# Kernel tuning notes

Measured on AMD Instinct MI355X. Metric: run time of the kernel, lower is better.

## Reference

```python
import jax, jax.numpy as jnp
import numpy as np

# NF4 codebook (bitsandbytes normal-float-4 values)
NF4 = jnp.asarray(np.array([
    -1.0, -0.6961928009986877, -0.5250730514526367, -0.39491748809814453,
    -0.28444138169288635, -0.18477343022823334, -0.09105003625154495, 0.0,
    0.07958029955625534, 0.16093020141124725, 0.24611230194568634, 0.33791524171829224,
    0.44070982933044434, 0.5626170039176941, 0.7229568362236023, 1.0], dtype=np.float32))

BLOCK = 64         # bnb nf4 blocksize
SCALING = 2.0      # alpha / r = 128 / 64
OUT, IN = 4096, 4096

def dequantize_nf4(codes, absmax):
    # codes: [out, in] int32 in [0,16); absmax: [out*in/BLOCK] per-block scale
    vals = NF4[codes].reshape(-1, BLOCK)           # [n_blocks, BLOCK]
    w = vals * absmax[:, None]                     # blockwise rescale
    return w.reshape(OUT, IN)                      # [out, in]

def setup_inputs() -> dict:
    key = jax.random.key(0)
    k1, k2, k3, k4, k5 = jax.random.split(key, 5)
    x = jax.random.normal(k1, (4, 2048, 4096), dtype=jnp.float32)
    lora_A = jax.random.normal(k2, (64, 4096), dtype=jnp.float32) * 0.02
    lora_B = jax.random.normal(k3, (4096, 64), dtype=jnp.float32) * 0.02
    absmax = jax.random.uniform(k4, (4096 * 4096 // BLOCK,), dtype=jnp.float32) * 0.1
    qweight_codes = jax.random.randint(k5, (4096, 4096), 0, 16, dtype=jnp.int32)
    return {"x": x, "lora_A": lora_A, "lora_B": lora_B,
            "absmax": absmax, "qweight_codes": qweight_codes}

def reference(x, lora_A, lora_B, absmax, qweight_codes):
    # LinearForward, quantized nf4 path, no dora/bone, dropout disabled (eval):
    # F.linear(x, W) + scaling * F.linear(F.linear(x, lora_A), lora_B)
    W = dequantize_nf4(qweight_codes, absmax)              # [out, in]
    base = jnp.einsum('btd,od->bto', x, W)                 # base GEMM
    lora = jnp.einsum('btr,or->bto', jnp.einsum('btd,rd->btr', x, lora_A), lora_B)
    return base + SCALING * lora
```

## Files before the change

kernel.cpp:

```cpp
#include <hip/hip_runtime.h>


typedef _Float16 half8 __attribute__((ext_vector_type(8)));
typedef float f32x4 __attribute__((ext_vector_type(4)));

#define M_DIM 8192
#define N_DIM 4096
#define K_DIM 4096

__constant__ float NF4C[16] = {
    -1.0f, -0.6961928009986877f, -0.5250730514526367f, -0.39491748809814453f,
    -0.28444138169288635f, -0.18477343022823334f, -0.09105003625154495f, 0.0f,
    0.07958029955625534f, 0.16093020141124725f, 0.24611230194568634f, 0.33791524171829224f,
    0.44070982933044434f, 0.5626170039176941f, 0.7229568362236023f, 1.0f};

__device__ __forceinline__ void gl16(void* lds, const void* g) {
  __builtin_amdgcn_global_load_lds(
      (const __attribute__((address_space(1))) void*)g,
      (__attribute__((address_space(3))) void*)lds, 16, 0, 0);
}

__global__ __launch_bounds__(256) void prep_x(const float4* __restrict__ x,
                                              half8* __restrict__ xh) {
  size_t i = (size_t)blockIdx.x * 256 + threadIdx.x;
  float4 a = x[2 * i];
  float4 b = x[2 * i + 1];
  half8 h;
  h[0] = (_Float16)a.x; h[1] = (_Float16)a.y; h[2] = (_Float16)a.z; h[3] = (_Float16)a.w;
  h[4] = (_Float16)b.x; h[5] = (_Float16)b.y; h[6] = (_Float16)b.z; h[7] = (_Float16)b.w;
  xh[i] = h;
}

#define PWP 132
__global__ __launch_bounds__(256) void prep_w(const float* __restrict__ lora_A,
                                              const float* __restrict__ lora_B,
                                              const float* __restrict__ absmax,
                                              const int* __restrict__ codes,
                                              _Float16* __restrict__ Wc) {
  __shared__ float At[64 * PWP];
  __shared__ float Bt[64 * PWP];
  __shared__ float nf4s[16];
  const int tid = threadIdx.x;
  const int bxi = blockIdx.x & 31;
  const int byo = blockIdx.x >> 5;
  const int i0 = bxi * 128;
  const int o0 = byo * 128;
  if (tid < 16) nf4s[tid] = NF4C[tid];
  for (int idx = tid; idx < 8192; idx += 256) {
    int r = idx >> 7, ii = idx & 127;
    At[r * PWP + ii] = lora_A[(size_t)r * 4096 + i0 + ii];
  }
  for (int idx = tid; idx < 8192; idx += 256) {
    int oo = idx >> 6, r = idx & 63;
    Bt[r * PWP + oo] = lora_B[(size_t)(o0 + oo) * 64 + r];
  }
  __syncthreads();
  const int tx = tid & 15;
  const int ty = tid >> 4;
  float accw[8][8];
#pragma unroll
  for (int i = 0; i < 8; ++i)
#pragma unroll
    for (int j = 0; j < 8; ++j) accw[i][j] = 0.0f;
  for (int r = 0; r < 64; ++r) {
    float4 a0 = *(const float4*)&At[r * PWP + tx * 8];
    float4 a1 = *(const float4*)&At[r * PWP + tx * 8 + 4];
    float4 b0 = *(const float4*)&Bt[r * PWP + ty * 8];
    float4 b1 = *(const float4*)&Bt[r * PWP + ty * 8 + 4];
    float av[8] = {a0.x, a0.y, a0.z, a0.w, a1.x, a1.y, a1.z, a1.w};
    float bv[8] = {b0.x, b0.y, b0.z, b0.w, b1.x, b1.y, b1.z, b1.w};
#pragma unroll
    for (int i = 0; i < 8; ++i)
#pragma unroll
      for (int j = 0; j < 8; ++j) accw[i][j] += bv[i] * av[j];
  }
#pragma unroll
  for (int i = 0; i < 8; ++i) {
    const int o_g = o0 + ty * 8 + i;
    const int* crow = codes + (size_t)o_g * 4096 + i0 + tx * 8;
    int4 c0 = *(const int4*)crow;
    int4 c1 = *(const int4*)(crow + 4);
    const float am = absmax[o_g * 64 + (i0 >> 6) + (tx >> 3)];
    half8 h;
    h[0] = (_Float16)(nf4s[c0.x] * am + 2.0f * accw[i][0]);
    h[1] = (_Float16)(nf4s[c0.y] * am + 2.0f * accw[i][1]);
    h[2] = (_Float16)(nf4s[c0.z] * am + 2.0f * accw[i][2]);
    h[3] = (_Float16)(nf4s[c0.w] * am + 2.0f * accw[i][3]);
    h[4] = (_Float16)(nf4s[c1.x] * am + 2.0f * accw[i][4]);
    h[5] = (_Float16)(nf4s[c1.y] * am + 2.0f * accw[i][5]);
    h[6] = (_Float16)(nf4s[c1.z] * am + 2.0f * accw[i][6]);
    h[7] = (_Float16)(nf4s[c1.w] * am + 2.0f * accw[i][7]);
    *(half8*)(Wc + (size_t)o_g * 4096 + i0 + tx * 8) = h;
  }
}

__global__ __launch_bounds__(256, 2) void gemm(const _Float16* __restrict__ Xh,
                                               const _Float16* __restrict__ Wc,
                                               float* __restrict__ out) {
  __shared__ _Float16 As[128 * 32];
  __shared__ _Float16 Bs[128 * 32];
  const int tid = threadIdx.x;
  const int lane = tid & 63;
  const int w = tid >> 6;
  const int bx = blockIdx.x & 31;
  const int by = blockIdx.x >> 5;
  const int wm = (w >> 1) * 64;
  const int wn = (w & 1) * 64;
  const int m16 = lane & 15;
  const int quad = lane >> 4;

  const int srow = w * 32 + (lane >> 2);
  const int scol = ((lane & 3) - (lane >> 3)) & 3;
  const _Float16* gA = Xh + (size_t)(by * 128 + srow) * K_DIM + scol * 8;
  const _Float16* gB = Wc + (size_t)(bx * 128 + srow) * K_DIM + scol * 8;
  _Float16* sA = As + w * 1024;
  _Float16* sB = Bs + w * 1024;

  const int fchunk = (quad + (m16 >> 1)) & 3;
  const _Float16* fa = As + (wm + m16) * 32 + fchunk * 8;
  const _Float16* fb = Bs + (wn + m16) * 32 + fchunk * 8;

  f32x4 acc[4][4];
#pragma unroll
  for (int mt = 0; mt < 4; ++mt)
#pragma unroll
    for (int nt = 0; nt < 4; ++nt) acc[mt][nt] = (f32x4){0.f, 0.f, 0.f, 0.f};

  for (int kt = 0; kt < K_DIM / 32; ++kt) {
    const _Float16* pa = gA + kt * 32;
    const _Float16* pb = gB + kt * 32;
    gl16(sA, pa);
    gl16(sA + 512, pa + 16 * K_DIM);
    gl16(sB, pb);
    gl16(sB + 512, pb + 16 * K_DIM);
    __syncthreads();
    half8 a0 = *(const half8*)(fa);
    half8 a1 = *(const half8*)(fa + 512);
    half8 a2 = *(const half8*)(fa + 1024);
    half8 a3 = *(const half8*)(fa + 1536);
    half8 b0 = *(const half8*)(fb);
    half8 b1 = *(const half8*)(fb + 512);
    half8 b2 = *(const half8*)(fb + 1024);
    half8 b3 = *(const half8*)(fb + 1536);
    acc[0][0] = __builtin_amdgcn_mfma_f32_16x16x32_f16(a0, b0, acc[0][0], 0, 0, 0);
    acc[0][1] = __builtin_amdgcn_mfma_f32_16x16x32_f16(a0, b1, acc[0][1], 0, 0, 0);
    acc[0][2] = __builtin_amdgcn_mfma_f32_16x16x32_f16(a0, b2, acc[0][2], 0, 0, 0);
    acc[0][3] = __builtin_amdgcn_mfma_f32_16x16x32_f16(a0, b3, acc[0][3], 0, 0, 0);
    acc[1][0] = __builtin_amdgcn_mfma_f32_16x16x32_f16(a1, b0, acc[1][0], 0, 0, 0);
    acc[1][1] = __builtin_amdgcn_mfma_f32_16x16x32_f16(a1, b1, acc[1][1], 0, 0, 0);
    acc[1][2] = __builtin_amdgcn_mfma_f32_16x16x32_f16(a1, b2, acc[1][2], 0, 0, 0);
    acc[1][3] = __builtin_amdgcn_mfma_f32_16x16x32_f16(a1, b3, acc[1][3], 0, 0, 0);
    acc[2][0] = __builtin_amdgcn_mfma_f32_16x16x32_f16(a2, b0, acc[2][0], 0, 0, 0);
    acc[2][1] = __builtin_amdgcn_mfma_f32_16x16x32_f16(a2, b1, acc[2][1], 0, 0, 0);
    acc[2][2] = __builtin_amdgcn_mfma_f32_16x16x32_f16(a2, b2, acc[2][2], 0, 0, 0);
    acc[2][3] = __builtin_amdgcn_mfma_f32_16x16x32_f16(a2, b3, acc[2][3], 0, 0, 0);
    acc[3][0] = __builtin_amdgcn_mfma_f32_16x16x32_f16(a3, b0, acc[3][0], 0, 0, 0);
    acc[3][1] = __builtin_amdgcn_mfma_f32_16x16x32_f16(a3, b1, acc[3][1], 0, 0, 0);
    acc[3][2] = __builtin_amdgcn_mfma_f32_16x16x32_f16(a3, b2, acc[3][2], 0, 0, 0);
    acc[3][3] = __builtin_amdgcn_mfma_f32_16x16x32_f16(a3, b3, acc[3][3], 0, 0, 0);
    __syncthreads();
  }

  const size_t rowbase = (size_t)by * 128 + wm + quad * 4;
  const int colbase = bx * 128 + wn + m16;
#pragma unroll
  for (int mt = 0; mt < 4; ++mt) {
#pragma unroll
    for (int r = 0; r < 4; ++r) {
      float* po = out + (rowbase + mt * 16 + r) * N_DIM + colbase;
      po[0]  = acc[mt][0][r];
      po[16] = acc[mt][1][r];
      po[32] = acc[mt][2][r];
      po[48] = acc[mt][3][r];
    }
  }
}

extern "C" void kernel_launch(void* const* d_in, const int* in_sizes, int n_in,
                              void* d_out, int out_size, void* d_ws, size_t ws_size,
                              hipStream_t stream) {
  const float* x      = (const float*)d_in[0];
  const float* lora_A = (const float*)d_in[1];
  const float* lora_B = (const float*)d_in[2];
  const float* absmax = (const float*)d_in[3];
  const int*   codes  = (const int*)d_in[4];
  float* out = (float*)d_out;

  _Float16* Xh = (_Float16*)d_ws;
  _Float16* Wc = Xh + (size_t)M_DIM * K_DIM;

  hipLaunchKernelGGL(prep_x, dim3((M_DIM * K_DIM) / (8 * 256)), dim3(256), 0, stream,
                     (const float4*)x, (half8*)Xh);
  hipLaunchKernelGGL(prep_w, dim3((N_DIM / 128) * (K_DIM / 128)), dim3(256), 0, stream,
                     lora_A, lora_B, absmax, codes, Wc);
  hipLaunchKernelGGL(gemm, dim3((N_DIM / 128) * (M_DIM / 128)), dim3(256), 0, stream,
                     Xh, Wc, out);
}
```

Measured before the change: 602.4 us.

## Rewrite GEMM as 256x256 tile, 512-thread double-buffered pipelined MFMA kernel

Result: faster. 522.3 us (-13.3%).

```diff
diff --git a/kernel.cpp b/kernel.cpp
--- a/kernel.cpp
+++ b/kernel.cpp
@@ -7,6 +7,7 @@
 #define M_DIM 8192
 #define N_DIM 4096
 #define K_DIM 4096
+#define NT (K_DIM / 64)
 
 __constant__ float NF4C[16] = {
     -1.0f, -0.6961928009986877f, -0.5250730514526367f, -0.39491748809814453f,
@@ -94,84 +95,139 @@
   }
 }
 
-__global__ __launch_bounds__(256, 2) void gemm(const _Float16* __restrict__ Xh,
+
+#define BAR __builtin_amdgcn_s_barrier()
+#define LGKM0 asm volatile("s_waitcnt lgkmcnt(0)" ::: "memory")
+
+__global__ __launch_bounds__(512, 2) void gemm(const _Float16* __restrict__ Xh,
                                                const _Float16* __restrict__ Wc,
                                                float* __restrict__ out) {
-  __shared__ _Float16 As[128 * 32];
-  __shared__ _Float16 Bs[128 * 32];
+  __shared__ _Float16 lds[65536];
   const int tid = threadIdx.x;
   const int lane = tid & 63;
   const int w = tid >> 6;
-  const int bx = blockIdx.x & 31;
-  const int by = blockIdx.x >> 5;
-  const int wm = (w >> 1) * 64;
-  const int wn = (w & 1) * 64;
+
+  const int swz = (blockIdx.x & 7) * 64 + (blockIdx.x >> 3);
+  const int by = swz >> 4;
+  const int bx = swz & 15;
+
   const int m16 = lane & 15;
   const int quad = lane >> 4;
-
-  const int srow = w * 32 + (lane >> 2);
-  const int scol = ((lane & 3) - (lane >> 3)) & 3;
-  const _Float16* gA = Xh + (size_t)(by * 128 + srow) * K_DIM + scol * 8;
-  const _Float16* gB = Wc + (size_t)(bx * 128 + srow) * K_DIM + scol * 8;
-  _Float16* sA = As + w * 1024;
-  _Float16* sB = Bs + w * 1024;
-
-  const int fchunk = (quad + (m16 >> 1)) & 3;
-  const _Float16* fa = As + (wm + m16) * 32 + fchunk * 8;
-  const _Float16* fb = Bs + (wn + m16) * 32 + fchunk * 8;
-
-  f32x4 acc[4][4];
-#pragma unroll
-  for (int mt = 0; mt < 4; ++mt)
-#pragma unroll
-    for (int nt = 0; nt < 4; ++nt) acc[mt][nt] = (f32x4){0.f, 0.f, 0.f, 0.f};
-
-  for (int kt = 0; kt < K_DIM / 32; ++kt) {
-    const _Float16* pa = gA + kt * 32;
-    const _Float16* pb = gB + kt * 32;
-    gl16(sA, pa);
-    gl16(sA + 512, pa + 16 * K_DIM);
-    gl16(sB, pb);
-    gl16(sB + 512, pb + 16 * K_DIM);
-    __syncthreads();
-    half8 a0 = *(const half8*)(fa);
-    half8 a1 = *(const half8*)(fa + 512);
-    half8 a2 = *(const half8*)(fa + 1024);
-    half8 a3 = *(const half8*)(fa + 1536);
-    half8 b0 = *(const half8*)(fb);
-    half8 b1 = *(const half8*)(fb + 512);
-    half8 b2 = *(const half8*)(fb + 1024);
-    half8 b3 = *(const half8*)(fb + 1536);
-    acc[0][0] = __builtin_amdgcn_mfma_f32_16x16x32_f16(a0, b0, acc[0][0], 0, 0, 0);
-    acc[0][1] = __builtin_amdgcn_mfma_f32_16x16x32_f16(a0, b1, acc[0][1], 0, 0, 0);
-    acc[0][2] = __builtin_amdgcn_mfma_f32_16x16x32_f16(a0, b2, acc[0][2], 0, 0, 0);
-    acc[0][3] = __builtin_amdgcn_mfma_f32_16x16x32_f16(a0, b3, acc[0][3], 0, 0, 0);
-    acc[1][0] = __builtin_amdgcn_mfma_f32_16x16x32_f16(a1, b0, acc[1][0], 0, 0, 0);
-    acc[1][1] = __builtin_amdgcn_mfma_f32_16x16x32_f16(a1, b1, acc[1][1], 0, 0, 0);
-    acc[1][2] = __builtin_amdgcn_mfma_f32_16x16x32_f16(a1, b2, acc[1][2], 0, 0, 0);
-    acc[1][3] = __builtin_amdgcn_mfma_f32_16x16x32_f16(a1, b3, acc[1][3], 0, 0, 0);
-    acc[2][0] = __builtin_amdgcn_mfma_f32_16x16x32_f16(a2, b0, acc[2][0], 0, 0, 0);
-    acc[2][1] = __builtin_amdgcn_mfma_f32_16x16x32_f16(a2, b1, acc[2][1], 0, 0, 0);
-    acc[2][2] = __builtin_amdgcn_mfma_f32_16x16x32_f16(a2, b2, acc[2][2], 0, 0, 0);
-    acc[2][3] = __builtin_amdgcn_mfma_f32_16x16x32_f16(a2, b3, acc[2][3], 0, 0, 0);
-    acc[3][0] = __builtin_amdgcn_mfma_f32_16x16x32_f16(a3, b0, acc[3][0], 0, 0, 0);
-    acc[3][1] = __builtin_amdgcn_mfma_f32_16x16x32_f16(a3, b1, acc[3][1], 0, 0, 0);
-    acc[3][2] = __builtin_amdgcn_mfma_f32_16x16x32_f16(a3, b2, acc[3][2], 0, 0, 0);
-    acc[3][3] = __builtin_amdgcn_mfma_f32_16x16x32_f16(a3, b3, acc[3][3], 0, 0, 0);
-    __syncthreads();
-  }
-
-  const size_t rowbase = (size_t)by * 128 + wm + quad * 4;
-  const int colbase = bx * 128 + wn + m16;
-#pragma unroll
-  for (int mt = 0; mt < 4; ++mt) {
+  const int csw = (quad ^ (m16 & 7)) * 8;
+  const int aoff0 = m16 * 64 + csw;
+  const int aoff1 = m16 * 64 + (csw ^ 32);
+  const int ha = w >> 2;
+  const int hboff = ((w & 3) >> 1) * 8192 + (w & 1) * 4096;
+
+  const int r0 = tid >> 3;
+  const int lc = (tid & 7) ^ (r0 & 7);
+  const _Float16* gAbase = Xh + (size_t)(by * 256 + r0) * K_DIM + lc * 8;
+  const _Float16* gBbase = Wc + (size_t)(bx * 256 + r0) * K_DIM + lc * 8;
+
+#define STAGE_A(H, BUF, T)                                                   \
+  do {                                                                       \
+    _Float16* d_ = lds + (BUF) * 32768 + (H) * 8192 + w * 512;               \
+    const _Float16* s_ = gAbase + (size_t)((H) * 128) * K_DIM + (T) * 64;    \
+    gl16(d_, s_);                                                            \
+    gl16(d_ + 4096, s_ + (size_t)64 * K_DIM);                                \
+  } while (0)
+#define STAGE_B(H, BUF, T)                                                   \
+  do {                                                                       \
+    _Float16* d_ = lds + (BUF) * 32768 + 16384 + (H) * 8192 + w * 512;       \
+    const _Float16* s_ = gBbase + (size_t)((H) * 128) * K_DIM + (T) * 64;    \
+    gl16(d_, s_);                                                            \
+    gl16(d_ + 4096, s_ + (size_t)64 * K_DIM);                                \
+  } while (0)
+
+  f32x4 acc[8][4];
+#pragma unroll
+  for (int m = 0; m < 8; ++m)
+#pragma unroll
+    for (int n = 0; n < 4; ++n) acc[m][n] = (f32x4){0.f, 0.f, 0.f, 0.f};
+
+  half8 af[4][2];
+  half8 bf[2][2];
+
+#define LOAD_A(MH)                                                           \
+  do {                                                                       \
+    _Pragma("unroll") for (int fm = 0; fm < 4; ++fm) {                       \
+      af[fm][0] = *(const half8*)(rA + (MH) * 4096 + fm * 1024 + aoff0);     \
+      af[fm][1] = *(const half8*)(rA + (MH) * 4096 + fm * 1024 + aoff1);     \
+    }                                                                        \
+  } while (0)
+#define LOAD_B(NH)                                                           \
+  do {                                                                       \
+    _Pragma("unroll") for (int fn = 0; fn < 2; ++fn) {                       \
+      bf[fn][0] = *(const half8*)(rBw + (NH) * 2048 + fn * 1024 + aoff0);    \
+      bf[fn][1] = *(const half8*)(rBw + (NH) * 2048 + fn * 1024 + aoff1);    \
+    }                                                                        \
+  } while (0)
+#define MFMA16(MH, NH)                                                       \
+  do {                                                                       \
+    __builtin_amdgcn_s_setprio(1);                                           \
+    _Pragma("unroll") for (int fm = 0; fm < 4; ++fm)                         \
+        _Pragma("unroll") for (int fn = 0; fn < 2; ++fn) {                   \
+      acc[(MH) * 4 + fm][(NH) * 2 + fn] = __builtin_amdgcn_mfma_f32_16x16x32_f16( \
+          af[fm][0], bf[fn][0], acc[(MH) * 4 + fm][(NH) * 2 + fn], 0, 0, 0); \
+      acc[(MH) * 4 + fm][(NH) * 2 + fn] = __builtin_amdgcn_mfma_f32_16x16x32_f16( \
+          af[fm][1], bf[fn][1], acc[(MH) * 4 + fm][(NH) * 2 + fn], 0, 0, 0); \
+    }                                                                        \
+    __builtin_amdgcn_s_setprio(0);                                           \
+  } while (0)
+
+  STAGE_A(0, 0, 0);
+  STAGE_A(1, 0, 0);
+  STAGE_B(0, 0, 0);
+  STAGE_B(1, 0, 0);
+  STAGE_A(0, 1, 1);
+  asm volatile("s_waitcnt vmcnt(2)" ::: "memory");
+  BAR;
+
+  for (int t = 0; t < NT; ++t) {
+    const int bsel = t & 1;
+    const int bn = bsel ^ 1;
+    const _Float16* rA = lds + bsel * 32768 + ha * 8192;
+    const _Float16* rBw = lds + bsel * 32768 + 16384 + hboff;
+    const bool more1 = (t + 1 < NT);
+    LOAD_A(0);
+    LOAD_B(0);
+    if (more1) STAGE_A(1, bn, t + 1);
+    BAR; LGKM0;
+    MFMA16(0, 0);
+    BAR;
+    LOAD_B(1);
+    if (more1) STAGE_B(0, bn, t + 1);
+    BAR; LGKM0;
+    MFMA16(0, 1);
+    BAR;
+    LOAD_A(1);
+    if (more1) STAGE_B(1, bn, t + 1);
+    BAR; LGKM0;
+    MFMA16(1, 1);
+    BAR;
+    LOAD_B(0);
+    if (t + 2 < NT) {
+      STAGE_A(0, bsel, t + 2);
+      asm volatile("s_waitcnt vmcnt(2)" ::: "memory");
+    } else {
+      asm volatile("s_waitcnt vmcnt(0)" ::: "memory");
+    }
+    BAR; LGKM0;
+    MFMA16(1, 0);
+    BAR;
+  }
+
+  const size_t rowbase = (size_t)by * 256 + ha * 128 + quad * 4;
+  const int colbase = bx * 256 + (w & 3) * 64 + m16;
+#pragma unroll
+  for (int m = 0; m < 8; ++m) {
 #pragma unroll
     for (int r = 0; r < 4; ++r) {
-      float* po = out + (rowbase + mt * 16 + r) * N_DIM + colbase;
-      po[0]  = acc[mt][0][r];
-      po[16] = acc[mt][1][r];
-      po[32] = acc[mt][2][r];
-      po[48] = acc[mt][3][r];
+      float* po = out + (rowbase + m * 16 + r) * N_DIM + colbase;
+      po[0]  = acc[m][0][r];
+      po[16] = acc[m][1][r];
+      po[32] = acc[m][2][r];
+      po[48] = acc[m][3][r];
     }
   }
 }
@@ -193,6 +249,6 @@
                      (const float4*)x, (half8*)Xh);
   hipLaunchKernelGGL(prep_w, dim3((N_DIM / 128) * (K_DIM / 128)), dim3(256), 0, stream,
                      lora_A, lora_B, absmax, codes, Wc);
-  hipLaunchKernelGGL(gemm, dim3((N_DIM / 128) * (M_DIM / 128)), dim3(256), 0, stream,
+  hipLaunchKernelGGL(gemm, dim3((M_DIM / 256) * (N_DIM / 256)), dim3(512), 0, stream,
                      Xh, Wc, out);
 }
```
